# Kernel optimization log

Measured on AMD Instinct MI355X. Metric: run time of the kernel, lower is better.

## Reference

```python
import jax, jax.numpy as jnp
import numpy as np

B, S, NB = 8, 512, 23
INIT, E, R, T = 512, 256, 3, 2
NEG = -9e8

def _gru(x, h, wih, whh, bih, bhh):
    gi = x @ wih.T + bih
    gh = h @ whh.T + bhh
    ir, iz, inn = jnp.split(gi, 3, axis=-1)
    hr, hz, hn = jnp.split(gh, 3, axis=-1)
    r = jax.nn.sigmoid(ir + hr)
    z = jax.nn.sigmoid(iz + hz)
    n = jnp.tanh(inn + r * hn)
    return (1.0 - z) * n + z * h

def setup_inputs():
    key = jax.random.key(0)
    ks = jax.random.split(key, 30)
    def lin(k, o, i):
        return jax.random.normal(k, (o, i), jnp.float32) * 0.02
    def vec(k, n):
        return jax.random.normal(k, (n,), jnp.float32) * 0.02
    inp = {}
    inp["amino_list"] = jax.random.normal(ks[0], (B, S, INIT), jnp.float32)
    inp["amino_mask"] = (jax.random.uniform(ks[1], (B, S)) < 0.9).astype(jnp.float32)
    inp["emb_W"] = lin(ks[2], E, INIT); inp["emb_b"] = vec(ks[3], E)
    inp["nb_W"] = lin(ks[4], E, INIT); inp["nb_b"] = vec(ks[5], E)
    inp["align_W"] = jax.random.normal(ks[6], (R, 1, 2 * E), jnp.float32) * 0.02
    inp["align_b"] = jax.random.normal(ks[7], (R, 1), jnp.float32) * 0.02
    inp["attend_W"] = jax.random.normal(ks[8], (R, E, E), jnp.float32) * 0.02
    inp["attend_b"] = jax.random.normal(ks[9], (R, E), jnp.float32) * 0.02
    inp["gru_wih"] = jax.random.normal(ks[10], (R, 3 * E, E), jnp.float32) * 0.02
    inp["gru_whh"] = jax.random.normal(ks[11], (R, 3 * E, E), jnp.float32) * 0.02
    inp["gru_bih"] = jax.random.normal(ks[12], (R, 3 * E), jnp.float32) * 0.02
    inp["gru_bhh"] = jax.random.normal(ks[13], (R, 3 * E), jnp.float32) * 0.02
    inp["seq_align_W"] = lin(ks[14], 1, 2 * E); inp["seq_align_b"] = vec(ks[15], 1)
    inp["seq_attend_W"] = lin(ks[16], E, E); inp["seq_attend_b"] = vec(ks[17], E)
    inp["seq_gru_wih"] = lin(ks[18], 3 * E, E); inp["seq_gru_bih"] = vec(ks[19], 3 * E)
    inp["seq_gru_whh"] = lin(ks[20], 3 * E, E); inp["seq_gru_bhh"] = vec(ks[21], 3 * E)
    inp["amino_degree_list"] = jax.random.randint(ks[22], (B, S, NB), -1, S)
    return inp

def reference(amino_list, amino_mask, emb_W, emb_b, nb_W, nb_b, align_W, align_b,
              attend_W, attend_b, gru_wih, gru_whh, gru_bih, gru_bhh,
              seq_align_W, seq_align_b, seq_attend_W, seq_attend_b,
              seq_gru_wih, seq_gru_whh, seq_gru_bih, seq_gru_bhh, amino_degree_list):
    idx = amino_degree_list
    lrelu = jax.nn.leaky_relu
    # per-batch neighbor gather: (S,D),(S,NB) -> (S,NB,D); index -1 wraps (masked out below)
    gather = jax.vmap(lambda f, i: f[i])
    feat = lrelu(amino_list @ emb_W.T + emb_b)               # (B,S,E)
    nfeat = lrelu(gather(amino_list, idx) @ nb_W.T + nb_b)   # (B,S,NB,E)
    attend_mask = (idx != -1).astype(feat.dtype)             # (B,S,NB)
    smask = jnp.where(idx == -1, NEG, 0.0).astype(feat.dtype)

    def attn(d, center, nbr):
        # align Linear on concat([center, nbr]) split into two matvecs (same math, no concat)
        aW = align_W[d, 0]
        score = lrelu(jnp.einsum('bse,e->bs', center, aW[:E])[:, :, None]
                      + jnp.einsum('bsne,e->bsn', nbr, aW[E:]) + align_b[d, 0])
        w = jax.nn.softmax(score + smask, axis=-1) * attend_mask   # softmax over neighbor axis
        nt = nbr @ attend_W[d].T + attend_b[d]
        return jax.nn.elu(jnp.einsum('bsn,bsne->bse', w, nt))

    h = _gru(attn(0, feat, nfeat).reshape(-1, E), feat.reshape(-1, E),
             gru_wih[0], gru_whh[0], gru_bih[0], gru_bhh[0])
    act = jax.nn.relu(h.reshape(B, S, E))
    for d in range(1, R):
        ctx = attn(d, act, gather(act, idx))
        h = _gru(ctx.reshape(-1, E), h, gru_wih[d], gru_whh[d], gru_bih[d], gru_bhh[d])
        act = jax.nn.relu(h.reshape(B, S, E))

    seq_feature = jnp.sum(act * amino_mask[:, :, None], axis=1)  # (B,E)
    act_mol = jax.nn.relu(seq_feature)                           # fixed across T (as in torch)
    seq_smask = jnp.where(amino_mask == 0, NEG, 0.0)
    saW = seq_align_W[0]
    act_seq = act_mol
    for _ in range(T):
        score = lrelu((act_mol @ saW[:E])[:, None]
                      + jnp.einsum('bse,e->bs', act, saW[E:]) + seq_align_b[0])
        w = jax.nn.softmax(score + seq_smask, axis=-1) * amino_mask  # softmax over seq axis
        tf = act @ seq_attend_W.T + seq_attend_b
        seq_ctx = jax.nn.elu(jnp.einsum('bs,bse->be', w, tf))
        seq_feature = _gru(seq_ctx, seq_feature, seq_gru_wih, seq_gru_whh, seq_gru_bih, seq_gru_bhh)
        act_seq = jax.nn.relu(seq_feature)
    return (act_seq, act)
```

## Files before the change

kernel.cpp:

```cpp
#include <hip/hip_runtime.h>
#include <math.h>


#define BSZ   8
#define SEQ   512
#define NBR   23
#define EMB   256
#define INITD 512
#define BS    (BSZ*SEQ)
#define G3    (3*EMB)
#define NEGV  -9e8f

typedef __attribute__((ext_vector_type(8))) short short8;
typedef __attribute__((ext_vector_type(4))) float f32x4;

__device__ __forceinline__ float lrelu(float x){ return x > 0.f ? x : 0.01f*x; }
__device__ __forceinline__ float elu1 (float x){ return x > 0.f ? x : (expf(x)-1.f); }
__device__ __forceinline__ float sigm (float x){ return 1.f/(1.f+expf(-x)); }
__device__ __forceinline__ float bf2f(ushort u){
    union { unsigned int i; float f; } v; v.i = ((unsigned int)u) << 16; return v.f;
}
__device__ __forceinline__ ushort f2bf(float f){
    union { float f; unsigned int i; } v; v.f = f;
    unsigned int u = v.i;
    return (ushort)((u + 0x7FFFu + ((u >> 16) & 1u)) >> 16);
}
__device__ __forceinline__ unsigned pk2(float a, float b){
    return (unsigned)f2bf(a) | ((unsigned)f2bf(b) << 16);
}
__device__ __forceinline__ void unpack8(uint4 v, float* o) {
    o[0]=bf2f((ushort)(v.x&0xffff)); o[1]=bf2f((ushort)(v.x>>16));
    o[2]=bf2f((ushort)(v.y&0xffff)); o[3]=bf2f((ushort)(v.y>>16));
    o[4]=bf2f((ushort)(v.z&0xffff)); o[5]=bf2f((ushort)(v.z>>16));
    o[6]=bf2f((ushort)(v.w&0xffff)); o[7]=bf2f((ushort)(v.w>>16));
}

__device__ __forceinline__ void gload_lds16(const void* g, void* l) {
    __builtin_amdgcn_global_load_lds(
        (const __attribute__((address_space(1))) unsigned int*)g,
        (__attribute__((address_space(3))) unsigned int*)l,
        16, 0, 0);
}

__global__ __launch_bounds__(256) void convert_flat(
    const float* __restrict__ amino, ushort* __restrict__ aminobf,
    const float* __restrict__ embW,  ushort* __restrict__ embWbf,
    const float* __restrict__ nbW,   ushort* __restrict__ nbWbf,
    const float* __restrict__ attW,  ushort* __restrict__ attWbf,
    const float* __restrict__ gwih,  ushort* __restrict__ gwihbf,
    const float* __restrict__ gwhh,  ushort* __restrict__ gwhhbf,
    const float* __restrict__ satW,  ushort* __restrict__ satWbf,
    const float* __restrict__ sgwih, ushort* __restrict__ sgwihbf,
    const float* __restrict__ sgwhh, ushort* __restrict__ sgwhhbf,
    float* __restrict__ seqfeatZ)
{
    const unsigned stride = gridDim.x * 256;
    for (unsigned u = blockIdx.x*256 + threadIdx.x; u < 524544u; u += stride) {
        const float* s; ushort* d; unsigned lu;
        if      (u < 262144u) { s=amino; d=aminobf; lu=u; }
        else if (u < 278528u) { s=embW;  d=embWbf;  lu=u-262144u; }
        else if (u < 294912u) { s=nbW;   d=nbWbf;   lu=u-278528u; }
        else if (u < 319488u) { s=attW;  d=attWbf;  lu=u-294912u; }
        else if (u < 393216u) { s=gwih;  d=gwihbf;  lu=u-319488u; }
        else if (u < 466944u) { s=gwhh;  d=gwhhbf;  lu=u-393216u; }
        else if (u < 475136u) { s=satW;  d=satWbf;  lu=u-466944u; }
        else if (u < 499712u) { s=sgwih; d=sgwihbf; lu=u-475136u; }
        else if (u < 524288u) { s=sgwhh; d=sgwhhbf; lu=u-499712u; }
        else {
            unsigned i = (u - 524288u) * 8;
            *reinterpret_cast<float4*>(&seqfeatZ[i])     = make_float4(0,0,0,0);
            *reinterpret_cast<float4*>(&seqfeatZ[i + 4]) = make_float4(0,0,0,0);
            continue;
        }
        size_t i = (size_t)lu * 8;
        float4 a = *reinterpret_cast<const float4*>(s + i);
        float4 b = *reinterpret_cast<const float4*>(s + i + 4);
        uint4 o;
        o.x = pk2(a.x, a.y); o.y = pk2(a.z, a.w);
        o.z = pk2(b.x, b.y); o.w = pk2(b.z, b.w);
        *reinterpret_cast<uint4*>(d + i) = o;
    }
}

struct GemmLds64 { ushort A[2][128][64]; ushort B[2][64][64]; };

template<int ACT>
__device__ __forceinline__ void gemm64_dev(
    const ushort* __restrict__ A, const ushort* __restrict__ W,
    const float* __restrict__ bias,
    float* __restrict__ C, ushort* __restrict__ Cbf,
    int N, int K, int bx, int by, GemmLds64& L)
{
    const int tid = threadIdx.x;
    const int m0 = bx * 128, n0 = by * 64;
    const int wv = tid >> 6, lane = tid & 63;
    const int fr = lane & 15, grp = lane >> 4;
    const int kc = K >> 3;
    const int mh = wv & 1, nh = wv >> 1;
    const int lrow = lane >> 3;
    const int csrc = (lane & 7) ^ lrow;

    f32x4 acc[4][2];
    #pragma unroll
    for (int i = 0; i < 4; ++i)
        #pragma unroll
        for (int n = 0; n < 2; ++n) acc[i][n] = (f32x4){0.f,0.f,0.f,0.f};

    auto stage = [&](int c, int k0) {
        const int kch = (k0 >> 3) + csrc;
        #pragma unroll
        for (int i = 0; i < 4; ++i) {
            const int s = (wv << 2) + i;
            gload_lds16(A + ((size_t)(m0 + (s << 3) + lrow) * kc + kch) * 8,
                        &L.A[c][s << 3][0]);
        }
        #pragma unroll
        for (int i = 0; i < 2; ++i) {
            const int s = (wv << 1) + i;
            gload_lds16(W + ((size_t)(n0 + (s << 3) + lrow) * kc + kch) * 8,
                        &L.B[c][s << 3][0]);
        }
    };
    auto compute = [&](int c) {
        #pragma unroll
        for (int ks = 0; ks < 2; ++ks) {
            short8 af[4];
            #pragma unroll
            for (int i = 0; i < 4; ++i) {
                const int ar = (mh << 6) + (i << 4) + fr;
                af[i] = *reinterpret_cast<const short8*>(
                    &L.A[c][ar][(((ks << 2) + grp) ^ (ar & 7)) << 3]);
            }
            #pragma unroll
            for (int n = 0; n < 2; ++n) {
                const int br = (nh << 5) + (n << 4) + fr;
                short8 bv = *reinterpret_cast<const short8*>(
                    &L.B[c][br][(((ks << 2) + grp) ^ (br & 7)) << 3]);
                #pragma unroll
                for (int i = 0; i < 4; ++i)
                    acc[i][n] = __builtin_amdgcn_mfma_f32_16x16x32_bf16(
                        af[i], bv, acc[i][n], 0, 0, 0);
            }
        }
    };

    const int KT = K >> 6;
    stage(0, 0);
    __syncthreads();
    int cur = 0;
    for (int kt = 1; kt < KT; ++kt) {
        stage(cur ^ 1, kt << 6);
        compute(cur);
        __syncthreads();
        cur ^= 1;
    }
    compute(cur);

    #pragma unroll
    for (int i = 0; i < 4; ++i) {
        const int mrow = m0 + (mh << 6) + (i << 4) + (grp << 2);
        #pragma unroll
        for (int n = 0; n < 2; ++n) {
            const int col = n0 + (nh << 5) + (n << 4) + fr;
            const float bv = bias[col];
            #pragma unroll
            for (int j = 0; j < 4; ++j) {
                float t = acc[i][n][j] + bv;
                if (ACT == 1) t = lrelu(t);
                size_t off = (size_t)(mrow + j) * N + col;
                if (C)   C[off] = t;
                if (Cbf) Cbf[off] = f2bf(t);
            }
        }
    }
}

__global__ __launch_bounds__(256) void featnbase_kernel(
    const ushort* __restrict__ aminobf,
    const ushort* __restrict__ embWbf, const float* __restrict__ embB,
    float* __restrict__ feat, ushort* __restrict__ featbf,
    const ushort* __restrict__ nbWbf, const float* __restrict__ nbB,
    float* __restrict__ nbase, ushort* __restrict__ nbasebf)
{
    __shared__ GemmLds64 L;
    int blk = blockIdx.x;
    if (blk < 128)
        gemm64_dev<1>(aminobf, embWbf, embB, feat, featbf, EMB, INITD, blk & 31, blk >> 5, L);
    else {
        blk -= 128;
        gemm64_dev<1>(aminobf, nbWbf, nbB, nbase, nbasebf, EMB, INITD, blk & 31, blk >> 5, L);
    }
}

__global__ __launch_bounds__(256) void dot2_kernel(
    const float* __restrict__ center, const float* __restrict__ nbrbase,
    const float* __restrict__ alignWd,
    float* __restrict__ cdot, float* __restrict__ ndot)
{
    const int lane = threadIdx.x & 63;
    const int wv   = threadIdx.x >> 6;
    const int e    = lane << 2;
    const int rb   = blockIdx.x * 32 + wv * 8;
    float4 w0 = *reinterpret_cast<const float4*>(&alignWd[e]);
    float4 w1 = *reinterpret_cast<const float4*>(&alignWd[EMB + e]);
    #pragma unroll
    for (int i = 0; i < 8; ++i) {
        const int r = rb + i;
        float4 xc = *reinterpret_cast<const float4*>(&center[(size_t)r*EMB + e]);
        float4 xn = *reinterpret_cast<const float4*>(&nbrbase[(size_t)r*EMB + e]);
        float ac = xc.x*w0.x + xc.y*w0.y + xc.z*w0.z + xc.w*w0.w;
        float an = xn.x*w1.x + xn.y*w1.y + xn.z*w1.z + xn.w*w1.w;
        #pragma unroll
        for (int off = 32; off; off >>= 1) {
            ac += __shfl_xor(ac, off, 64);
            an += __shfl_xor(an, off, 64);
        }
        if (lane == 0) { cdot[r] = ac; ndot[r] = an; }
    }
}

struct GALds { ushort ctxpre[16][256]; ushort ctx[16][256]; float wsum_s[16]; };

__global__ __launch_bounds__(512) void gatherattend_kernel(
    const float* __restrict__ cdot, const float* __restrict__ ndot,
    const int* __restrict__ idx, const ushort* __restrict__ nbr,
    const float* __restrict__ alignBd,
    const ushort* __restrict__ attWd, const float* __restrict__ attBd,
    ushort* __restrict__ ctxbf)
{
    __shared__ GALds L;
    const int tid = threadIdx.x;
    const int r0 = blockIdx.x * 16;

    {
        const int row16 = tid >> 5, sub = tid & 31;
        const int r = r0 + row16, b = r >> 9;
        float sc = -3e38f, vm = 0.f; int rn = 0;
        if (sub < NBR) {
            int j = idx[(size_t)r*NBR + sub];
            int valid = (j >= 0);
            int jj = valid ? j : j + SEQ;
            rn = b*SEQ + jj;
            vm = (float)valid;
            sc = lrelu(cdot[r] + ndot[rn] + alignBd[0]) + (valid ? 0.f : NEGV);
        }
        float m = sc;
        #pragma unroll
        for (int off = 16; off; off >>= 1) m = fmaxf(m, __shfl_xor(m, off, 32));
        float ev = (sub < NBR) ? expf(sc - m) : 0.f;
        float s = ev;
        #pragma unroll
        for (int off = 16; off; off >>= 1) s += __shfl_xor(s, off, 32);
        float wgt = ev * vm / s;
        float ws = wgt;
        #pragma unroll
        for (int off = 16; off; off >>= 1) ws += __shfl_xor(ws, off, 32);
        float a8[8] = {};
        const int e0 = sub << 3;
        #pragma unroll
        for (int n = 0; n < NBR; ++n) {
            float wn = __shfl(wgt, n, 32);
            int   rr = __shfl(rn, n, 32);
            uint4 v = *reinterpret_cast<const uint4*>(&nbr[(size_t)rr*EMB + e0]);
            float x[8]; unpack8(v, x);
            #pragma unroll
            for (int i = 0; i < 8; ++i) a8[i] += wn * x[i];
        }
        uint4 o;
        o.x = pk2(a8[0],a8[1]); o.y = pk2(a8[2],a8[3]);
        o.z = pk2(a8[4],a8[5]); o.w = pk2(a8[6],a8[7]);
        *reinterpret_cast<uint4*>(&L.ctxpre[row16][(sub ^ (row16&7)) << 3]) = o;
        if (sub == 0) L.wsum_s[row16] = ws;
    }
    __syncthreads();

    const int wv = tid >> 6, lane = tid & 63;
    const int fr = lane & 15, grp = lane >> 4;
    {
        f32x4 acc[2] = {(f32x4){0,0,0,0},(f32x4){0,0,0,0}};
        #pragma unroll
        for (int kt = 0; kt < 8; ++kt) {
            short8 af = *reinterpret_cast<const short8*>(
                &L.ctxpre[fr][((((kt<<2)+grp) ^ (fr&7)) << 3)]);
            #pragma unroll
            for (int f = 0; f < 2; ++f) {
                const int col = (wv<<5) + (f<<4) + fr;
                short8 bv = *reinterpret_cast<const short8*>(
                    &attWd[(size_t)col*EMB + (kt<<5) + (grp<<3)]);
                acc[f] = __builtin_amdgcn_mfma_f32_16x16x32_bf16(af, bv, acc[f], 0, 0, 0);
            }
        }
        #pragma unroll
        for (int f = 0; f < 2; ++f) {
            const int col = (wv<<5) + (f<<4) + fr;
            const float bb = attBd[col];
            #pragma unroll
            for (int j = 0; j < 4; ++j) {
                const int row = (grp<<2) + j;
                L.ctx[row][col] = f2bf(elu1(acc[f][j] + L.wsum_s[row]*bb));
            }
        }
    }
    __syncthreads();
    {
        const int row = tid >> 5, c = tid & 31;
        uint4 v = *reinterpret_cast<const uint4*>(&L.ctx[row][c << 3]);
        *reinterpret_cast<uint4*>(&ctxbf[(size_t)(r0+row)*EMB + (c << 3)]) = v;
    }
}

__global__ __launch_bounds__(256) void gigh_kernel(
    const ushort* __restrict__ ctxbf, const ushort* __restrict__ gwihd,
    const float* __restrict__ gbihd, ushort* __restrict__ gibf,
    const ushort* __restrict__ hprevbf, const ushort* __restrict__ gwhhd,
    const float* __restrict__ gbhhd, ushort* __restrict__ ghbf)
{
    __shared__ GemmLds64 L;
    int blk = blockIdx.x;
    if (blk < 384)
        gemm64_dev<0>(ctxbf, gwihd, gbihd, nullptr, gibf, G3, EMB, blk & 31, blk >> 5, L);
    else {
        blk -= 384;
        gemm64_dev<0>(hprevbf, gwhhd, gbhhd, nullptr, ghbf, G3, EMB, blk & 31, blk >> 5, L);
    }
}

template<int LAST>
__global__ __launch_bounds__(512) void grudot_kernel(
    const ushort* __restrict__ gibf, const ushort* __restrict__ ghbf,
    const ushort* __restrict__ hprevbf, const float* __restrict__ nextW,
    const float* __restrict__ mask,
    ushort* __restrict__ hbf, float* __restrict__ actout,
    ushort* __restrict__ actbf,
    float* __restrict__ cdotO, float* __restrict__ ndotO,
    float* __restrict__ seqfeatA)
{
    __shared__ float sred[16][256];
    const int tid = threadIdx.x;
    const int row = tid >> 5, sub = tid & 31;
    const int e0 = sub << 3;
    const size_t r = (size_t)blockIdx.x * 16 + row;
    const size_t gb = r*G3;
    uint4 giA = *reinterpret_cast<const uint4*>(&gibf[gb + e0]);
    uint4 giB = *reinterpret_cast<const uint4*>(&gibf[gb + 256 + e0]);
    uint4 giC = *reinterpret_cast<const uint4*>(&gibf[gb + 512 + e0]);
    uint4 ghA = *reinterpret_cast<const uint4*>(&ghbf[gb + e0]);
    uint4 ghB = *reinterpret_cast<const uint4*>(&ghbf[gb + 256 + e0]);
    uint4 ghC = *reinterpret_cast<const uint4*>(&ghbf[gb + 512 + e0]);
    uint4 hpv = *reinterpret_cast<const uint4*>(&hprevbf[r*EMB + e0]);
    float ir_[8], iz_[8], in_[8], hr_[8], hz_[8], hn_[8], hp_[8];
    unpack8(giA, ir_); unpack8(giB, iz_); unpack8(giC, in_);
    unpack8(ghA, hr_); unpack8(ghB, hz_); unpack8(ghC, hn_);
    unpack8(hpv, hp_);
    float hv8[8], av8[8];
    #pragma unroll
    for (int i = 0; i < 8; ++i) {
        float rg = sigm(ir_[i] + hr_[i]);
        float z  = sigm(iz_[i] + hz_[i]);
        float n  = tanhf(in_[i] + rg*hn_[i]);
        hv8[i] = (1.f - z)*n + z*hp_[i];
        av8[i] = fmaxf(hv8[i], 0.f);
    }
    if (LAST) {
        *reinterpret_cast<float4*>(&actout[r*EMB + e0])     = make_float4(av8[0],av8[1],av8[2],av8[3]);
        *reinterpret_cast<float4*>(&actout[r*EMB + e0 + 4]) = make_float4(av8[4],av8[5],av8[6],av8[7]);
    }
    uint4 hb, ab;
    hb.x = pk2(hv8[0],hv8[1]); hb.y = pk2(hv8[2],hv8[3]);
    hb.z = pk2(hv8[4],hv8[5]); hb.w = pk2(hv8[6],hv8[7]);
    ab.x = pk2(av8[0],av8[1]); ab.y = pk2(av8[2],av8[3]);
    ab.z = pk2(av8[4],av8[5]); ab.w = pk2(av8[6],av8[7]);
    *reinterpret_cast<uint4*>(&hbf[r*EMB + e0])   = hb;
    *reinterpret_cast<uint4*>(&actbf[r*EMB + e0]) = ab;
    float pc = 0.f, pn = 0.f;
    float4 w1a = *reinterpret_cast<const float4*>(&nextW[EMB + e0]);
    float4 w1b = *reinterpret_cast<const float4*>(&nextW[EMB + e0 + 4]);
    pn = av8[0]*w1a.x + av8[1]*w1a.y + av8[2]*w1a.z + av8[3]*w1a.w
       + av8[4]*w1b.x + av8[5]*w1b.y + av8[6]*w1b.z + av8[7]*w1b.w;
    if (!LAST) {
        float4 w0a = *reinterpret_cast<const float4*>(&nextW[e0]);
        float4 w0b = *reinterpret_cast<const float4*>(&nextW[e0 + 4]);
        pc = av8[0]*w0a.x + av8[1]*w0a.y + av8[2]*w0a.z + av8[3]*w0a.w
           + av8[4]*w0b.x + av8[5]*w0b.y + av8[6]*w0b.z + av8[7]*w0b.w;
    }
    #pragma unroll
    for (int off = 16; off; off >>= 1) {
        pn += __shfl_xor(pn, off, 32);
        if (!LAST) pc += __shfl_xor(pc, off, 32);
    }
    if (sub == 0) {
        if (!LAST) cdotO[r] = pc;
        ndotO[r] = pn;
    }
    if (LAST) {
        const float mk = mask[r];
        #pragma unroll
        for (int i = 0; i < 8; ++i) sred[row][e0 + i] = av8[i] * mk;
        __syncthreads();
        if (tid < 256) {
            float s = 0.f;
            #pragma unroll
            for (int rr = 0; rr < 16; ++rr) s += sred[rr][tid];
            atomicAdd(&seqfeatA[(blockIdx.x >> 5)*EMB + tid], s);
        }
    }
}

__global__ __launch_bounds__(256) void seqpre_kernel(
    const ushort* __restrict__ actbf, const ushort* __restrict__ satWbf,
    const float* __restrict__ satB, float* __restrict__ tf)
{
    __shared__ GemmLds64 L;
    gemm64_dev<0>(actbf, satWbf, satB, tf, nullptr, EMB, EMB,
                  blockIdx.x & 31, blockIdx.x >> 5, L);
}

__global__ __launch_bounds__(256) void seqpv2_kernel(
    const float* __restrict__ ad, const float* __restrict__ mask,
    const float* __restrict__ saB, const float* __restrict__ saW,
    const float* __restrict__ seqfeat, const float* __restrict__ tf,
    float* __restrict__ partial)
{
    const int st = blockIdx.x, b = blockIdx.y;
    const int tid = threadIdx.x;
    __shared__ float w_s[SEQ];
    __shared__ float red[256];
    red[tid] = fmaxf(seqfeat[b*EMB + tid], 0.f) * saW[tid];
    __syncthreads();
    for (int off = 128; off; off >>= 1) {
        if (tid < off) red[tid] += red[tid + off];
        __syncthreads();
    }
    const float cb = red[0];
    __syncthreads();
    float mk0 = mask[b*SEQ + tid], mk1 = mask[b*SEQ + 256 + tid];
    float bb = saB[0];
    float s0 = lrelu(cb + ad[b*SEQ + tid] + bb)       + (mk0 == 0.f ? NEGV : 0.f);
    float s1 = lrelu(cb + ad[b*SEQ + 256 + tid] + bb) + (mk1 == 0.f ? NEGV : 0.f);
    red[tid] = fmaxf(s0, s1); __syncthreads();
    for (int off = 128; off; off >>= 1) {
        if (tid < off) red[tid] = fmaxf(red[tid], red[tid + off]);
        __syncthreads();
    }
    float m = red[0]; __syncthreads();
    float e0 = expf(s0 - m), e1 = expf(s1 - m);
    red[tid] = e0 + e1; __syncthreads();
    for (int off = 128; off; off >>= 1) {
        if (tid < off) red[tid] += red[tid + off];
        __syncthreads();
    }
    float inv = 1.f / red[0];
    w_s[tid]       = e0 * inv * mk0;
    w_s[tid + 256] = e1 * inv * mk1;
    __syncthreads();
    float acc = 0.f;
    const int s0i = st * 32;
    #pragma unroll 4
    for (int s = s0i; s < s0i + 32; ++s)
        acc += w_s[s] * tf[((size_t)b*SEQ + s)*EMB + tid];
    partial[((size_t)b*16 + st)*EMB + tid] = acc;
}

template<int T0>
__global__ __launch_bounds__(512) void seqstep_kernel(
    const float* __restrict__ partial, const float* __restrict__ sfin,
    const ushort* __restrict__ sgwihbf, const float* __restrict__ sgbih,
    const ushort* __restrict__ sgwhhbf, const float* __restrict__ sgbhh,
    float* __restrict__ sgi, float* __restrict__ sfout,
    float* __restrict__ actseq)
{
    const int b = blockIdx.x >> 2, q = blockIdx.x & 3;
    const int tid = threadIdx.x, lane = tid & 63, wv = tid >> 6;
    __shared__ float xs[EMB];
    __shared__ float hs[EMB];
    __shared__ float gis[192], ghs[192];
    if (tid < EMB) {
        hs[tid] = sfin[b*EMB + tid];
        if (T0) {
            float a = 0.f;
            #pragma unroll
            for (int st = 0; st < 16; ++st)
                a += partial[((size_t)b*16 + st)*EMB + tid];
            xs[tid] = elu1(a);
        }
    }
    if (!T0) {
        for (int l = tid; l < 192; l += 512) {
            int g = (l >> 6)*EMB + (q << 6) + (l & 63);
            gis[l] = sgi[b*G3 + g];
        }
    }
    __syncthreads();
    const int nrows = T0 ? 384 : 192;
    const int rpw = nrows >> 3;
    for (int i = 0; i < rpw; ++i) {
        const int l = wv * rpw + i;
        const int iswih = T0 && (l < 192);
        const int ll = (T0 && l >= 192) ? l - 192 : l;
        const int g = (ll >> 6)*EMB + (q << 6) + (ll & 63);
        const ushort* Wm = iswih ? sgwihbf : sgwhhbf;
        ushort4 w4 = *reinterpret_cast<const ushort4*>(&Wm[(size_t)g*EMB + (lane << 2)]);
        float4 x4 = *reinterpret_cast<const float4*>(iswih ? &xs[lane << 2] : &hs[lane << 2]);
        float d = bf2f(w4.x)*x4.x + bf2f(w4.y)*x4.y + bf2f(w4.z)*x4.z + bf2f(w4.w)*x4.w;
        #pragma unroll
        for (int off = 32; off; off >>= 1) d += __shfl_xor(d, off, 64);
        if (lane == 0) {
            if (iswih) {
                d += sgbih[g];
                gis[ll] = d;
                sgi[b*G3 + g] = d;
            } else {
                ghs[ll] = d + sgbhh[g];
            }
        }
    }
    __syncthreads();
    if (tid < 64) {
        const int e = (q << 6) + tid;
        float rg = sigm(gis[tid]       + ghs[tid]);
        float z  = sigm(gis[64 + tid]  + ghs[64 + tid]);
        float n  = tanhf(gis[128 + tid] + rg*ghs[128 + tid]);
        float hv = (1.f - z)*n + z*hs[e];
        sfout[b*EMB + e]  = hv;
        actseq[b*EMB + e] = fmaxf(hv, 0.f);
    }
}

extern "C" void kernel_launch(void* const* d_in, const int* in_sizes, int n_in,
                              void* d_out, int out_size, void* d_ws, size_t ws_size,
                              hipStream_t stream) {
    (void)in_sizes; (void)n_in; (void)out_size; (void)ws_size;
    const float* amino  = (const float*)d_in[0];
    const float* mask   = (const float*)d_in[1];
    const float* embW   = (const float*)d_in[2];
    const float* embB   = (const float*)d_in[3];
    const float* nbW    = (const float*)d_in[4];
    const float* nbB    = (const float*)d_in[5];
    const float* alignW = (const float*)d_in[6];
    const float* alignB = (const float*)d_in[7];
    const float* attW   = (const float*)d_in[8];
    const float* attB   = (const float*)d_in[9];
    const float* gwih   = (const float*)d_in[10];
    const float* gwhh   = (const float*)d_in[11];
    const float* gbih   = (const float*)d_in[12];
    const float* gbhh   = (const float*)d_in[13];
    const float* saW    = (const float*)d_in[14];
    const float* saB    = (const float*)d_in[15];
    const float* satW   = (const float*)d_in[16];
    const float* satB   = (const float*)d_in[17];
    const float* sgwih  = (const float*)d_in[18];
    const float* sgbih  = (const float*)d_in[19];
    const float* sgwhh  = (const float*)d_in[20];
    const float* sgbhh  = (const float*)d_in[21];
    const int*   idx    = (const int*)d_in[22];

    char* cur = (char*)d_ws;
    auto alloc = [&](size_t bytes) -> char* {
        char* p = cur; cur += (bytes + 255) & ~(size_t)255; return p;
    };
    float* feat    = (float*)alloc((size_t)BS*EMB*4);
    float* nbase   = (float*)alloc((size_t)BS*EMB*4);
    float* tf      = (float*)alloc((size_t)BS*EMB*4);
    float* cdot    = (float*)alloc(BS*4);
    float* ndot    = (float*)alloc(BS*4);
    float* seqfeat = (float*)alloc(BSZ*EMB*4);
    float* sf2     = (float*)alloc(BSZ*EMB*4);
    float* sgi     = (float*)alloc(BSZ*G3*4);
    float* partial = (float*)alloc((size_t)BSZ*16*EMB*4);
    ushort* aminobf  = (ushort*)alloc((size_t)BS*INITD*2);
    ushort* featbf   = (ushort*)alloc((size_t)BS*EMB*2);
    ushort* nbasebf  = (ushort*)alloc((size_t)BS*EMB*2);
    ushort* actbf    = (ushort*)alloc((size_t)BS*EMB*2);
    ushort* hbf      = (ushort*)alloc((size_t)BS*EMB*2);
    ushort* ctxbf    = (ushort*)alloc((size_t)BS*EMB*2);
    ushort* gibf     = (ushort*)alloc((size_t)BS*G3*2);
    ushort* ghbf     = (ushort*)alloc((size_t)BS*G3*2);
    ushort* embWbf   = (ushort*)alloc((size_t)EMB*INITD*2);
    ushort* nbWbf    = (ushort*)alloc((size_t)EMB*INITD*2);
    ushort* attWbf   = (ushort*)alloc((size_t)3*EMB*EMB*2);
    ushort* gwihbf   = (ushort*)alloc((size_t)3*G3*EMB*2);
    ushort* gwhhbf   = (ushort*)alloc((size_t)3*G3*EMB*2);
    ushort* satWbf   = (ushort*)alloc((size_t)EMB*EMB*2);
    ushort* sgwihbf  = (ushort*)alloc((size_t)G3*EMB*2);
    ushort* sgwhhbf  = (ushort*)alloc((size_t)G3*EMB*2);

    float* out    = (float*)d_out;
    float* actseq = out;
    float* act    = out + BSZ*EMB;

    convert_flat<<<2048, 256, 0, stream>>>(
        amino, aminobf, embW, embWbf, nbW, nbWbf, attW, attWbf,
        gwih, gwihbf, gwhh, gwhhbf, satW, satWbf,
        sgwih, sgwihbf, sgwhh, sgwhhbf, seqfeat);

    featnbase_kernel<<<256, 256, 0, stream>>>(
        aminobf, embWbf, embB, feat, featbf, nbWbf, nbB, nbase, nbasebf);

    dot2_kernel<<<128, 256, 0, stream>>>(feat, nbase, alignW, cdot, ndot);

    for (int d = 0; d < 3; ++d) {
        const ushort* nbrbf   = (d == 0) ? nbasebf : actbf;
        const ushort* hprevbf = (d == 0) ? featbf  : hbf;
        gatherattend_kernel<<<BS/16, 512, 0, stream>>>(
            cdot, ndot, idx, nbrbf, alignB + d,
            attWbf + (size_t)d*EMB*EMB, attB + d*EMB, ctxbf);
        gigh_kernel<<<768, 256, 0, stream>>>(
            ctxbf, gwihbf + (size_t)d*G3*EMB, gbih + d*G3, gibf,
            hprevbf, gwhhbf + (size_t)d*G3*EMB, gbhh + d*G3, ghbf);
        if (d < 2) {
            grudot_kernel<0><<<BS/16, 512, 0, stream>>>(
                gibf, ghbf, hprevbf, alignW + (d+1)*2*EMB, mask,
                hbf, act, actbf, cdot, ndot, seqfeat);
        } else {
            grudot_kernel<1><<<BS/16, 512, 0, stream>>>(
                gibf, ghbf, hprevbf, saW, mask,
                hbf, act, actbf, cdot, ndot, seqfeat);
        }
    }

    seqpre_kernel<<<128, 256, 0, stream>>>(actbf, satWbf, satB, tf);
    seqpv2_kernel<<<dim3(16, BSZ), 256, 0, stream>>>(
        ndot, mask, saB, saW, seqfeat, tf, partial);
    seqstep_kernel<1><<<32, 512, 0, stream>>>(
        partial, seqfeat, sgwihbf, sgbih, sgwhhbf, sgbhh, sgi, sf2, actseq);
    seqstep_kernel<0><<<32, 512, 0, stream>>>(
        partial, sf2, sgwihbf, sgbih, sgwhhbf, sgbhh, sgi, seqfeat, actseq);
}
```

Baseline: 164.7 us.

## Overlap gh GEMM with gather-attend and fuse seq attend GEMM into pooling

The hidden-state GEMM (gh) now runs in the same launch as the gather-attend blocks, with their LDS shared through a union and gather-attend reshaped to 256 threads. The gi GEMM gets its own launch after that. The sequence attend projection (tf) is now computed per block with MFMA inside the pooling kernel, which removes the fp32 tf buffer and one launch. The costs are lower parallelism per gather-attend block and a pooling kernel with much larger LDS use (about 49 KB), which may limit occupancy on a grid of only 128 blocks.

```diff
diff --git a/kernel.cpp b/kernel.cpp
--- a/kernel.cpp
+++ b/kernel.cpp
@@ -220,20 +220,22 @@
 }
 
 struct GALds { ushort ctxpre[16][256]; ushort ctx[16][256]; float wsum_s[16]; };
-
-__global__ __launch_bounds__(512) void gatherattend_kernel(
+union RoundLds { GALds ga; GemmLds64 g; };
+
+__device__ __forceinline__ void gatherattend_dev(
+    int blk,
     const float* __restrict__ cdot, const float* __restrict__ ndot,
     const int* __restrict__ idx, const ushort* __restrict__ nbr,
     const float* __restrict__ alignBd,
     const ushort* __restrict__ attWd, const float* __restrict__ attBd,
-    ushort* __restrict__ ctxbf)
-{
-    __shared__ GALds L;
+    ushort* __restrict__ ctxbf, GALds& L)
+{
     const int tid = threadIdx.x;
-    const int r0 = blockIdx.x * 16;
-
-    {
-        const int row16 = tid >> 5, sub = tid & 31;
+    const int r0 = blk * 16;
+
+    #pragma unroll
+    for (int half = 0; half < 2; ++half) {
+        const int row16 = (tid >> 5) + half*8, sub = tid & 31;
         const int r = r0 + row16, b = r >> 9;
         float sc = -3e38f, vm = 0.f; int rn = 0;
         if (sub < NBR) {
@@ -277,22 +279,24 @@
     const int wv = tid >> 6, lane = tid & 63;
     const int fr = lane & 15, grp = lane >> 4;
     {
-        f32x4 acc[2] = {(f32x4){0,0,0,0},(f32x4){0,0,0,0}};
+        f32x4 acc[4];
+        #pragma unroll
+        for (int f = 0; f < 4; ++f) acc[f] = (f32x4){0,0,0,0};
         #pragma unroll
         for (int kt = 0; kt < 8; ++kt) {
             short8 af = *reinterpret_cast<const short8*>(
                 &L.ctxpre[fr][((((kt<<2)+grp) ^ (fr&7)) << 3)]);
             #pragma unroll
-            for (int f = 0; f < 2; ++f) {
-                const int col = (wv<<5) + (f<<4) + fr;
+            for (int f = 0; f < 4; ++f) {
+                const int col = (wv<<6) + (f<<4) + fr;
                 short8 bv = *reinterpret_cast<const short8*>(
                     &attWd[(size_t)col*EMB + (kt<<5) + (grp<<3)]);
                 acc[f] = __builtin_amdgcn_mfma_f32_16x16x32_bf16(af, bv, acc[f], 0, 0, 0);
             }
         }
         #pragma unroll
-        for (int f = 0; f < 2; ++f) {
-            const int col = (wv<<5) + (f<<4) + fr;
+        for (int f = 0; f < 4; ++f) {
+            const int col = (wv<<6) + (f<<4) + fr;
             const float bb = attBd[col];
             #pragma unroll
             for (int j = 0; j < 4; ++j) {
@@ -303,26 +307,42 @@
     }
     __syncthreads();
     {
-        const int row = tid >> 5, c = tid & 31;
-        uint4 v = *reinterpret_cast<const uint4*>(&L.ctx[row][c << 3]);
-        *reinterpret_cast<uint4*>(&ctxbf[(size_t)(r0+row)*EMB + (c << 3)]) = v;
-    }
-}
-
-__global__ __launch_bounds__(256) void gigh_kernel(
-    const ushort* __restrict__ ctxbf, const ushort* __restrict__ gwihd,
-    const float* __restrict__ gbihd, ushort* __restrict__ gibf,
+        #pragma unroll
+        for (int half = 0; half < 2; ++half) {
+            const int row = (tid >> 5) + half*8, c = tid & 31;
+            uint4 v = *reinterpret_cast<const uint4*>(&L.ctx[row][c << 3]);
+            *reinterpret_cast<uint4*>(&ctxbf[(size_t)(r0+row)*EMB + (c << 3)]) = v;
+        }
+    }
+}
+
+__global__ __launch_bounds__(256) void gagh_kernel(
+    const float* __restrict__ cdot, const float* __restrict__ ndot,
+    const int* __restrict__ idx, const ushort* __restrict__ nbr,
+    const float* __restrict__ alignBd,
+    const ushort* __restrict__ attWd, const float* __restrict__ attBd,
+    ushort* __restrict__ ctxbf,
     const ushort* __restrict__ hprevbf, const ushort* __restrict__ gwhhd,
     const float* __restrict__ gbhhd, ushort* __restrict__ ghbf)
 {
+    __shared__ RoundLds L;
+    if (blockIdx.x < 256) {
+        gatherattend_dev(blockIdx.x, cdot, ndot, idx, nbr, alignBd,
+                         attWd, attBd, ctxbf, L.ga);
+    } else {
+        int blk = blockIdx.x - 256;
+        gemm64_dev<0>(hprevbf, gwhhd, gbhhd, nullptr, ghbf,
+                      G3, EMB, blk & 31, blk >> 5, L.g);
+    }
+}
+
+__global__ __launch_bounds__(256) void gi_kernel(
+    const ushort* __restrict__ ctxbf, const ushort* __restrict__ gwihd,
+    const float* __restrict__ gbihd, ushort* __restrict__ gibf)
+{
     __shared__ GemmLds64 L;
-    int blk = blockIdx.x;
-    if (blk < 384)
-        gemm64_dev<0>(ctxbf, gwihd, gbihd, nullptr, gibf, G3, EMB, blk & 31, blk >> 5, L);
-    else {
-        blk -= 384;
-        gemm64_dev<0>(hprevbf, gwhhd, gbhhd, nullptr, ghbf, G3, EMB, blk & 31, blk >> 5, L);
-    }
+    gemm64_dev<0>(ctxbf, gwihd, gbihd, nullptr, gibf, G3, EMB,
+                  blockIdx.x & 31, blockIdx.x >> 5, L);
 }
 
 template<int LAST>
@@ -406,25 +426,30 @@
     }
 }
 
-__global__ __launch_bounds__(256) void seqpre_kernel(
-    const ushort* __restrict__ actbf, const ushort* __restrict__ satWbf,
-    const float* __restrict__ satB, float* __restrict__ tf)
-{
-    __shared__ GemmLds64 L;
-    gemm64_dev<0>(actbf, satWbf, satB, tf, nullptr, EMB, EMB,
-                  blockIdx.x & 31, blockIdx.x >> 5, L);
-}
-
-__global__ __launch_bounds__(256) void seqpv2_kernel(
+__global__ __launch_bounds__(256) void seqpvtf_kernel(
     const float* __restrict__ ad, const float* __restrict__ mask,
     const float* __restrict__ saB, const float* __restrict__ saW,
-    const float* __restrict__ seqfeat, const float* __restrict__ tf,
+    const float* __restrict__ seqfeat,
+    const ushort* __restrict__ actbf, const ushort* __restrict__ satWbf,
+    const float* __restrict__ satB,
     float* __restrict__ partial)
 {
     const int st = blockIdx.x, b = blockIdx.y;
     const int tid = threadIdx.x;
+    __shared__ ushort As[32][256];
+    __shared__ float tf_s[32][256];
     __shared__ float w_s[SEQ];
     __shared__ float red[256];
+    const int r0 = b*SEQ + st*32;
+
+    {
+        #pragma unroll
+        for (int i = 0; i < 4; ++i) {
+            const int row = (tid >> 5) + i*8, c = tid & 31;
+            uint4 v = *reinterpret_cast<const uint4*>(&actbf[(size_t)(r0+row)*EMB + (c<<3)]);
+            *reinterpret_cast<uint4*>(&As[row][(c ^ (row&7)) << 3]) = v;
+        }
+    }
     red[tid] = fmaxf(seqfeat[b*EMB + tid], 0.f) * saW[tid];
     __syncthreads();
     for (int off = 128; off; off >>= 1) {
@@ -443,22 +468,65 @@
         __syncthreads();
     }
     float m = red[0]; __syncthreads();
-    float e0 = expf(s0 - m), e1 = expf(s1 - m);
-    red[tid] = e0 + e1; __syncthreads();
+    float e0v = expf(s0 - m), e1v = expf(s1 - m);
+    red[tid] = e0v + e1v; __syncthreads();
     for (int off = 128; off; off >>= 1) {
         if (tid < off) red[tid] += red[tid + off];
         __syncthreads();
     }
     float inv = 1.f / red[0];
-    w_s[tid]       = e0 * inv * mk0;
-    w_s[tid + 256] = e1 * inv * mk1;
-    __syncthreads();
-    float acc = 0.f;
-    const int s0i = st * 32;
-    #pragma unroll 4
-    for (int s = s0i; s < s0i + 32; ++s)
-        acc += w_s[s] * tf[((size_t)b*SEQ + s)*EMB + tid];
-    partial[((size_t)b*16 + st)*EMB + tid] = acc;
+    w_s[tid]       = e0v * inv * mk0;
+    w_s[tid + 256] = e1v * inv * mk1;
+    __syncthreads();
+
+    {
+        const int wv = tid >> 6, lane = tid & 63;
+        const int fr = lane & 15, grp = lane >> 4;
+        f32x4 acc[2][4];
+        #pragma unroll
+        for (int mt = 0; mt < 2; ++mt)
+            #pragma unroll
+            for (int f = 0; f < 4; ++f) acc[mt][f] = (f32x4){0,0,0,0};
+        #pragma unroll
+        for (int kt = 0; kt < 8; ++kt) {
+            short8 af[2];
+            #pragma unroll
+            for (int mt = 0; mt < 2; ++mt) {
+                const int ar = (mt << 4) + fr;
+                af[mt] = *reinterpret_cast<const short8*>(
+                    &As[ar][((((kt<<2)+grp) ^ (ar&7)) << 3)]);
+            }
+            #pragma unroll
+            for (int f = 0; f < 4; ++f) {
+                const int col = (wv<<6) + (f<<4) + fr;
+                short8 bv = *reinterpret_cast<const short8*>(
+                    &satWbf[(size_t)col*EMB + (kt<<5) + (grp<<3)]);
+                #pragma unroll
+                for (int mt = 0; mt < 2; ++mt)
+                    acc[mt][f] = __builtin_amdgcn_mfma_f32_16x16x32_bf16(
+                        af[mt], bv, acc[mt][f], 0, 0, 0);
+            }
+        }
+        #pragma unroll
+        for (int f = 0; f < 4; ++f) {
+            const int col = (wv<<6) + (f<<4) + fr;
+            const float bias = satB[col];
+            #pragma unroll
+            for (int mt = 0; mt < 2; ++mt)
+                #pragma unroll
+                for (int j = 0; j < 4; ++j)
+                    tf_s[(mt<<4) + (grp<<2) + j][col] = acc[mt][f][j] + bias;
+        }
+    }
+    __syncthreads();
+    {
+        float acc = 0.f;
+        const int s0i = st * 32;
+        #pragma unroll 4
+        for (int s = 0; s < 32; ++s)
+            acc += w_s[s0i + s] * tf_s[s][tid];
+        partial[((size_t)b*16 + st)*EMB + tid] = acc;
+    }
 }
 
 template<int T0>
@@ -560,7 +628,6 @@
     };
     float* feat    = (float*)alloc((size_t)BS*EMB*4);
     float* nbase   = (float*)alloc((size_t)BS*EMB*4);
-    float* tf      = (float*)alloc((size_t)BS*EMB*4);
     float* cdot    = (float*)alloc(BS*4);
     float* ndot    = (float*)alloc(BS*4);
     float* seqfeat = (float*)alloc(BSZ*EMB*4);
@@ -601,12 +668,12 @@
     for (int d = 0; d < 3; ++d) {
         const ushort* nbrbf   = (d == 0) ? nbasebf : actbf;
         const ushort* hprevbf = (d == 0) ? featbf  : hbf;
-        gatherattend_kernel<<<BS/16, 512, 0, stream>>>(
+        gagh_kernel<<<640, 256, 0, stream>>>(
             cdot, ndot, idx, nbrbf, alignB + d,
-            attWbf + (size_t)d*EMB*EMB, attB + d*EMB, ctxbf);
-        gigh_kernel<<<768, 256, 0, stream>>>(
-            ctxbf, gwihbf + (size_t)d*G3*EMB, gbih + d*G3, gibf,
+            attWbf + (size_t)d*EMB*EMB, attB + d*EMB, ctxbf,
             hprevbf, gwhhbf + (size_t)d*G3*EMB, gbhh + d*G3, ghbf);
+        gi_kernel<<<384, 256, 0, stream>>>(
+            ctxbf, gwihbf + (size_t)d*G3*EMB, gbih + d*G3, gibf);
         if (d < 2) {
             grudot_kernel<0><<<BS/16, 512, 0, stream>>>(
                 gibf, ghbf, hprevbf, alignW + (d+1)*2*EMB, mask,
@@ -618,9 +685,8 @@
         }
     }
 
-    seqpre_kernel<<<128, 256, 0, stream>>>(actbf, satWbf, satB, tf);
-    seqpv2_kernel<<<dim3(16, BSZ), 256, 0, stream>>>(
-        ndot, mask, saB, saW, seqfeat, tf, partial);
+    seqpvtf_kernel<<<dim3(16, BSZ), 256, 0, stream>>>(
+        ndot, mask, saB, saW, seqfeat, actbf, satWbf, satB, partial);
     seqstep_kernel<1><<<32, 512, 0, stream>>>(
         partial, seqfeat, sgwihbf, sgbih, sgwhhbf, sgbhh, sgi, sf2, actseq);
     seqstep_kernel<0><<<32, 512, 0, stream>>>(
```

Measured after the change: 173.9 us. 1.06x slower.
